# Performance work log

Measured on AMD Instinct MI355X. Metric: run time of the kernel, lower is better.

The kernel has to match this reference:

```python
import jax, jax.numpy as jnp
import numpy as np

N_NODES = 20000
N_EDGES = 320000
N_GRAPHS = 512
HEADS1 = 10
C1 = 78   # per-head out channels of gcn1
C2 = 100  # out channels of gcn2 (heads=1)
NEG_SLOPE = 0.2


def setup_inputs() -> dict:
    key = jax.random.key(0)
    ks = jax.random.split(key, 16)
    glorot = lambda k, shp: jax.random.normal(k, shp, jnp.float32) * np.sqrt(2.0 / (shp[0] + shp[-1]))
    x = jax.random.normal(ks[0], (N_NODES, 78), jnp.float32)
    edge_index = jax.random.randint(ks[1], (2, N_EDGES), 0, N_NODES, jnp.int64)
    batch = jnp.sort(jax.random.randint(ks[2], (N_NODES,), 0, N_GRAPHS, jnp.int64))
    return {
        "x": x,
        "edge_index": edge_index,
        "batch": batch,
        "num_graphs": N_GRAPHS,
        "W1": glorot(ks[3], (78, HEADS1 * C1)),
        "a_src1": glorot(ks[4], (HEADS1, C1)),
        "a_dst1": glorot(ks[5], (HEADS1, C1)),
        "b1": jnp.zeros((HEADS1 * C1,), jnp.float32),
        "W2": glorot(ks[6], (HEADS1 * C1, C2)),
        "a_src2": glorot(ks[7], (1, C2)),
        "a_dst2": glorot(ks[8], (1, C2)),
        "b2": jnp.zeros((C2,), jnp.float32),
        "Wg": glorot(ks[9], (C2, C2)),
        "bg": jnp.zeros((C2,), jnp.float32),
    }


def gat_conv(x, src, dst, W, a_src, a_dst, b, heads, out_ch):
    """PyG-style GATConv (concat=True, add_self_loops already applied, eval mode)."""
    N = x.shape[0]
    h = (x @ W).reshape(N, heads, out_ch)          # [N,H,C]
    alpha_s = jnp.einsum('nhc,hc->nh', h, a_src)   # [N,H]
    alpha_d = jnp.einsum('nhc,hc->nh', h, a_dst)
    e = jax.nn.leaky_relu(alpha_s[src] + alpha_d[dst], NEG_SLOPE)  # [E,H]
    # segment softmax over destination nodes
    m = jax.ops.segment_max(e, dst, num_segments=N)                # [N,H]
    e = jnp.exp(e - m[dst])
    denom = jax.ops.segment_sum(e, dst, num_segments=N)
    alpha = e / (denom[dst] + 1e-16)                               # [E,H]
    out = jax.ops.segment_sum(h[src] * alpha[:, :, None], dst, num_segments=N)
    return out.reshape(N, heads * out_ch) + b


def reference(x, edge_index, batch, num_graphs, W1, a_src1, a_dst1, b1,
              W2, a_src2, a_dst2, b2, Wg, bg):
    N = x.shape[0]
    # add self loops (PyG GATConv default)
    loops = jnp.arange(N, dtype=edge_index.dtype)
    src = jnp.concatenate([edge_index[0], loops])
    dst = jnp.concatenate([edge_index[1], loops])
    h = gat_conv(x, src, dst, W1, a_src1, a_dst1, b1, HEADS1, C1)   # [N,780]
    h = jax.nn.elu(h)
    h = gat_conv(h, src, dst, W2, a_src2, a_dst2, b2, 1, C2)        # [N,100]
    h = jax.nn.relu(h)
    g = jax.ops.segment_max(h, batch, num_segments=num_graphs)      # [G,100] global max pool
    g = jax.nn.relu(g @ Wg + bg)
    return g
```

## Files before the change

### kernel.cpp

```cpp
#include <hip/hip_runtime.h>
#include <hip/hip_bf16.h>

#define N_NODES  20000
#define N_EDGES  320000
#define E_TOT    (N_EDGES + N_NODES)
#define N_GRAPHS 512
#define H1 10
#define C1 78
#define F1 780
#define C2 100
#define NEG_SLOPE 0.2f
#define KSPLIT 5
#define K1PAD 96
#define K2PAD 800
#define K2CHUNK 160
#define AP1 104
#define AP2 40
#define HP 12

typedef short bf16x8 __attribute__((ext_vector_type(8)));
typedef float f32x4 __attribute__((ext_vector_type(4)));
typedef _Float16 half2v __attribute__((ext_vector_type(2)));
typedef unsigned short ushort_t;

__device__ __forceinline__ float bf_lo(unsigned int u) { return __uint_as_float(u << 16); }
__device__ __forceinline__ float bf_hi(unsigned int u) { return __uint_as_float(u & 0xFFFF0000u); }
__device__ __forceinline__ ushort_t f2b(float v) {
  __hip_bfloat16 b = __float2bfloat16(v);
  return *reinterpret_cast<ushort_t*>(&b);
}
__device__ __forceinline__ ushort_t f2h(float v) {
  _Float16 h = (_Float16)v;
  return *reinterpret_cast<ushort_t*>(&h);
}
__device__ __forceinline__ float lrelu(float v) { return (v > 0.f) ? v : NEG_SLOPE * v; }
__device__ __forceinline__ float dot2h(unsigned int a, unsigned int b, float c) {
  union { unsigned int u; half2v v; } A, B;
  A.u = a; B.u = b;
  return __builtin_amdgcn_fdot2(A.v, B.v, c, false);
}


__global__ void k_count(const int* __restrict__ ei, int* __restrict__ cnt) {
  int e = blockIdx.x * blockDim.x + threadIdx.x;
  if (e >= E_TOT) return;
  int dst = (e < N_EDGES) ? ei[N_EDGES + e] : (e - N_EDGES);
  atomicAdd(&cnt[dst], 1);
}

__global__ __launch_bounds__(1024) void k_scan(const int* __restrict__ cnt,
                                               int* __restrict__ offs, int n) {
  const int PER = 20;
  int t = threadIdx.x;
  int lane = t & 63, wv = t >> 6;
  int base = t * PER;
  int loc[PER];
  int run = 0;
#pragma unroll
  for (int k = 0; k < PER; k++) {
    int idx = base + k;
    int v = (idx < n) ? cnt[idx] : 0;
    run += v;
    loc[k] = run;
  }
  int total = run;
  int sc = total;
#pragma unroll
  for (int o = 1; o < 64; o <<= 1) {
    int u = __shfl_up(sc, o);
    if (lane >= o) sc += u;
  }
  __shared__ int ws[16];
  if (lane == 63) ws[wv] = sc;
  __syncthreads();
  if (t == 0) {
    int r = 0;
#pragma unroll
    for (int i = 0; i < 16; i++) { int v = ws[i]; ws[i] = r; r += v; }
  }
  __syncthreads();
  int excl = ws[wv] + sc - total;
#pragma unroll
  for (int k = 0; k < PER; k++) {
    int idx = base + k;
    if (idx < n) offs[idx + 1] = excl + loc[k];
  }
  if (t == 0) offs[0] = 0;
}

__global__ void k_scatter(const int* __restrict__ ei, const int* __restrict__ offs,
                          int* __restrict__ cursor, int* __restrict__ srcs,
                          int* __restrict__ dsts) {
  int e = blockIdx.x * blockDim.x + threadIdx.x;
  if (e >= E_TOT) return;
  int src, dst;
  if (e < N_EDGES) { src = ei[e]; dst = ei[N_EDGES + e]; }
  else             { src = dst = e - N_EDGES; }
  int pos = offs[dst] + atomicAdd(&cursor[dst], 1);
  srcs[pos] = src;
  dsts[pos] = dst;
}


#define PR0 (2 * H1 * C1)
#define PR1 (H1 * 80 * K1PAD)
#define PR2 (112 * K2PAD)
#define PR3 (N_NODES * (K2PAD - F1))
#define PR4 (N_NODES * 40)

__global__ void k_prep(const float* __restrict__ W1, const float* __restrict__ a_src,
                       const float* __restrict__ a_dst, const float* __restrict__ W2,
                       const float* __restrict__ x,
                       float* __restrict__ Vs, float* __restrict__ Vd,
                       ushort_t* __restrict__ W1t, ushort_t* __restrict__ W2t,
                       ushort_t* __restrict__ hab, ushort_t* __restrict__ xhf) {
  int t = blockIdx.x * blockDim.x + threadIdx.x;
  if (t < PR0) {
    int which = (t >= H1 * C1) ? 1 : 0;
    int r = t - which * H1 * C1;
    int h = r / C1, k = r - h * C1;
    const float* a = which ? a_dst : a_src;
    float s = 0.f;
    for (int c = 0; c < C1; c++) s += W1[(size_t)k * F1 + h * C1 + c] * a[h * C1 + c];
    (which ? Vd : Vs)[h * C1 + k] = s;
    return;
  }
  t -= PR0;
  if (t < PR1) {
    int h = t / (80 * K1PAD);
    int rem = t - h * 80 * K1PAD;
    int c = rem / K1PAD, k = rem - c * K1PAD;
    float v = (c < C1 && k < C1) ? W1[(size_t)k * F1 + h * C1 + c] : 0.f;
    W1t[t] = f2b(v);
    return;
  }
  t -= PR1;
  if (t < PR2) {
    int c = t / K2PAD, k = t - c * K2PAD;
    float v = (c < C2 && k < F1) ? W2[(size_t)k * C2 + c] : 0.f;
    W2t[t] = f2b(v);
    return;
  }
  t -= PR2;
  if (t < PR3) {
    int n = t / (K2PAD - F1), j = t - n * (K2PAD - F1);
    hab[(size_t)n * K2PAD + F1 + j] = 0;
    return;
  }
  t -= PR3;
  if (t < PR4) {
    int n = t / 40, c2 = t - n * 40;
    ushort2 o;
    if (c2 < 39) { o.x = f2h(x[(size_t)n * C1 + 2 * c2]); o.y = f2h(x[(size_t)n * C1 + 2 * c2 + 1]); }
    else         { o.x = 0; o.y = 0; }
    *(ushort2*)(xhf + (size_t)n * 80 + 2 * c2) = o;
  }
}


__global__ __launch_bounds__(256) void k_alpha1x(const float* __restrict__ x,
                                                 const float* __restrict__ Vs,
                                                 const float* __restrict__ Vd,
                                                 float* __restrict__ asb,
                                                 float* __restrict__ adb) {
  __shared__ float sVs[H1 * C1], sVd[H1 * C1];
  for (int i = threadIdx.x; i < H1 * C1; i += 256) { sVs[i] = Vs[i]; sVd[i] = Vd[i]; }
  __syncthreads();
  int t = blockIdx.x * 256 + threadIdx.x;
  if (t >= N_NODES * H1) return;
  int n = t / H1, h = t - n * H1;
  const float2* row = (const float2*)(x + (size_t)n * C1);
  const float2* vs2 = (const float2*)(sVs + h * C1);
  const float2* vd2 = (const float2*)(sVd + h * C1);
  float s0 = 0.f, s1 = 0.f;
#pragma unroll 13
  for (int i = 0; i < C1 / 2; i++) {
    float2 v = row[i];
    float2 a = vs2[i];
    float2 b = vd2[i];
    s0 += v.x * a.x + v.y * a.y;
    s1 += v.x * b.x + v.y * b.y;
  }
  asb[(size_t)n * HP + h] = s0;
  adb[(size_t)n * HP + h] = s1;
}


__global__ void k_ex1(const float* __restrict__ asb, const float* __restrict__ adb,
                      const int* __restrict__ srcs, const int* __restrict__ dsts,
                      ushort_t* __restrict__ ex1t) {
  int e = blockIdx.x * blockDim.x + threadIdx.x;
  if (e >= E_TOT) return;
  int s = srcs[e], d = dsts[e];
  const float* pa = asb + (size_t)s * HP;
  const float* pd = adb + (size_t)d * HP;
  float4 a0 = *(const float4*)pa, a1 = *(const float4*)(pa + 4);
  float2 a2 = *(const float2*)(pa + 8);
  float4 d0 = *(const float4*)pd, d1 = *(const float4*)(pd + 4);
  float2 d2 = *(const float2*)(pd + 8);
  float r[10];
  r[0] = __expf(lrelu(a0.x + d0.x)); r[1] = __expf(lrelu(a0.y + d0.y));
  r[2] = __expf(lrelu(a0.z + d0.z)); r[3] = __expf(lrelu(a0.w + d0.w));
  r[4] = __expf(lrelu(a1.x + d1.x)); r[5] = __expf(lrelu(a1.y + d1.y));
  r[6] = __expf(lrelu(a1.z + d1.z)); r[7] = __expf(lrelu(a1.w + d1.w));
  r[8] = __expf(lrelu(a2.x + d2.x)); r[9] = __expf(lrelu(a2.y + d2.y));
#pragma unroll
  for (int h = 0; h < H1; h++) ex1t[(size_t)h * E_TOT + e] = f2h(r[h]);
}


__global__ __launch_bounds__(256) void k_aggv5(const ushort_t* __restrict__ xhf,
                                               const ushort_t* __restrict__ ex1t,
                                               const int* __restrict__ offs,
                                               const int* __restrict__ srcs,
                                               ushort_t* __restrict__ xb) {
  int wid = (blockIdx.x * 256 + threadIdx.x) >> 6;
  int lane = threadIdx.x & 63;
  if (wid >= N_NODES) return;
  int n = wid;
  int beg = __builtin_amdgcn_readfirstlane(offs[n]);
  int end = __builtin_amdgcn_readfirstlane(offs[n + 1]);

  float acc0[H1] = {}, acc1[H1] = {}, sum[H1] = {};
  const unsigned int ONES = 0x3C003C00u;

  for (int e0 = beg & ~1; e0 < end; e0 += 2) {
    unsigned int m = 0xFFFFFFFFu;
    if (e0 < beg) m &= 0xFFFF0000u;
    if (e0 + 1 >= end) m &= 0x0000FFFFu;
    int s0 = srcs[e0], s1 = srcs[e0 + 1];
    unsigned int w[H1];
#pragma unroll
    for (int h = 0; h < H1; h++)
      w[h] = *(const unsigned int*)(ex1t + (size_t)h * E_TOT + e0);
    unsigned int xv0 = 0, xv1 = 0;
    if (lane < 39) {
      xv0 = *(const unsigned int*)(xhf + (size_t)s0 * 80 + 2 * lane);
      xv1 = *(const unsigned int*)(xhf + (size_t)s1 * 80 + 2 * lane);
    }
    unsigned int xA = __builtin_amdgcn_perm(xv1, xv0, 0x05040100u) & m;
    unsigned int xB = __builtin_amdgcn_perm(xv1, xv0, 0x07060302u) & m;
    unsigned int on = ONES & m;
#pragma unroll
    for (int h = 0; h < H1; h++) {
      acc0[h] = dot2h(w[h], xA, acc0[h]);
      acc1[h] = dot2h(w[h], xB, acc1[h]);
      sum[h]  = dot2h(w[h], on, sum[h]);
    }
  }

  if (lane < 48) {
    int colu = (lane < 39) ? 2 * lane : C1 + 2 * (lane - 39);
#pragma unroll
    for (int h = 0; h < H1; h++) {
      float iv = 1.f / (sum[h] + 1e-16f);
      ushort2 o;
      if (lane < 39) { o.x = f2b(acc0[h] * iv); o.y = f2b(acc1[h] * iv); }
      else           { o.x = 0; o.y = 0; }
      *(ushort2*)(xb + ((size_t)h * N_NODES + n) * K1PAD + colu) = o;
    }
  }
}


__global__ __launch_bounds__(256) void k_bgemm_m(const ushort_t* __restrict__ xb,
                                                 const ushort_t* __restrict__ W1t,
                                                 const float* __restrict__ b1,
                                                 ushort_t* __restrict__ hab) {
  __shared__ ushort_t sA[64 * AP1];
  __shared__ ushort_t sB[80 * AP1];
  int h = blockIdx.y;
  int m0 = blockIdx.x * 64;
  int tid = threadIdx.x;

  for (int i = tid; i < 64 * 12; i += 256) {
    int r = i / 12, cx = i - r * 12;
    uint4 v = make_uint4(0, 0, 0, 0);
    int m = m0 + r;
    if (m < N_NODES) v = *(const uint4*)(xb + ((size_t)h * N_NODES + m) * K1PAD + cx * 8);
    *(uint4*)(sA + r * AP1 + cx * 8) = v;
  }
  for (int i = tid; i < 80 * 12; i += 256) {
    int c = i / 12, cx = i - c * 12;
    uint4 v = *(const uint4*)(W1t + ((size_t)h * 80 + c) * K1PAD + cx * 8);
    *(uint4*)(sB + c * AP1 + cx * 8) = v;
  }
  __syncthreads();

  int w = tid >> 6, l = tid & 63;
  int rb = l & 15, g = l >> 4;
  f32x4 acc[5] = {};
  const ushort_t* pa = sA + (w * 16 + rb) * AP1 + g * 8;
#pragma unroll
  for (int k0 = 0; k0 < K1PAD; k0 += 32) {
    bf16x8 a = *(const bf16x8*)(pa + k0);
#pragma unroll
    for (int ct = 0; ct < 5; ct++) {
      bf16x8 b = *(const bf16x8*)(sB + (ct * 16 + rb) * AP1 + k0 + g * 8);
      acc[ct] = __builtin_amdgcn_mfma_f32_16x16x32_bf16(a, b, acc[ct], 0, 0, 0);
    }
  }

  int mrow = m0 + w * 16 + g * 4;
#pragma unroll
  for (int ct = 0; ct < 5; ct++) {
    int col = ct * 16 + rb;
    if (col >= C1) continue;
    float bias = b1[h * C1 + col];
#pragma unroll
    for (int r = 0; r < 4; r++) {
      int m = mrow + r;
      if (m >= N_NODES) continue;
      float v = acc[ct][r] + bias;
      v = (v > 0.f) ? v : (__expf(v) - 1.f);
      hab[(size_t)m * K2PAD + h * C1 + col] = f2b(v);
    }
  }
}


__global__ __launch_bounds__(256) void k_gemm2m(const ushort_t* __restrict__ hab,
                                                const ushort_t* __restrict__ W2t,
                                                float* __restrict__ part) {
  __shared__ ushort_t sA[64 * AP2];
  __shared__ ushort_t sB[112 * AP2];
  int m0 = blockIdx.x * 64;
  int kz = blockIdx.y * K2CHUNK;
  int tid = threadIdx.x;
  int w = tid >> 6, l = tid & 63;
  int rb = l & 15, g = l >> 4;
  f32x4 acc[7] = {};

  for (int ks = 0; ks < K2CHUNK; ks += 32) {
    int kbase = kz + ks;
    {
      int r = tid >> 2, cx = tid & 3;
      uint4 v = make_uint4(0, 0, 0, 0);
      int m = m0 + r;
      if (m < N_NODES) v = *(const uint4*)(hab + (size_t)m * K2PAD + kbase + cx * 8);
      *(uint4*)(sA + r * AP2 + cx * 8) = v;
    }
    for (int i = tid; i < 112 * 4; i += 256) {
      int c = i >> 2, cx = i & 3;
      uint4 v = *(const uint4*)(W2t + (size_t)c * K2PAD + kbase + cx * 8);
      *(uint4*)(sB + c * AP2 + cx * 8) = v;
    }
    __syncthreads();
    bf16x8 a = *(const bf16x8*)(sA + (w * 16 + rb) * AP2 + g * 8);
#pragma unroll
    for (int ct = 0; ct < 7; ct++) {
      bf16x8 b = *(const bf16x8*)(sB + (ct * 16 + rb) * AP2 + g * 8);
      acc[ct] = __builtin_amdgcn_mfma_f32_16x16x32_bf16(a, b, acc[ct], 0, 0, 0);
    }
    __syncthreads();
  }

  float* P = part + (size_t)blockIdx.y * N_NODES * C2;
  int mrow = m0 + w * 16 + g * 4;
#pragma unroll
  for (int ct = 0; ct < 7; ct++) {
    int col = ct * 16 + rb;
    if (col >= C2) continue;
#pragma unroll
    for (int r = 0; r < 4; r++) {
      int m = mrow + r;
      if (m < N_NODES) P[(size_t)m * C2 + col] = acc[ct][r];
    }
  }
}


__global__ __launch_bounds__(256) void k_redalpha(const float* __restrict__ part,
                                                  const float* __restrict__ a_src,
                                                  const float* __restrict__ a_dst,
                                                  ushort_t* __restrict__ z2b,
                                                  float* __restrict__ as2,
                                                  float* __restrict__ ad2) {
  int wid = (blockIdx.x * 256 + threadIdx.x) >> 6;
  int lane = threadIdx.x & 63;
  if (wid >= N_NODES) return;
  float ps = 0.f, pd = 0.f;
  if (lane < C2 / 2) {
    float2 s = make_float2(0.f, 0.f);
#pragma unroll
    for (int c = 0; c < KSPLIT; c++) {
      float2 v = *(const float2*)(part + (size_t)c * N_NODES * C2 + (size_t)wid * C2 + 2 * lane);
      s.x += v.x; s.y += v.y;
    }
    ushort2 o; o.x = f2b(s.x); o.y = f2b(s.y);
    *(ushort2*)(z2b + (size_t)wid * C2 + 2 * lane) = o;
    ps = s.x * a_src[2 * lane] + s.y * a_src[2 * lane + 1];
    pd = s.x * a_dst[2 * lane] + s.y * a_dst[2 * lane + 1];
  }
#pragma unroll
  for (int o = 32; o; o >>= 1) { ps += __shfl_xor(ps, o); pd += __shfl_xor(pd, o); }
  if (lane == 0) { as2[wid] = ps; ad2[wid] = pd; }
}


__global__ void k_ex2(const float* __restrict__ as2, const float* __restrict__ ad2,
                      const int* __restrict__ srcs, const int* __restrict__ dsts,
                      float* __restrict__ ex2) {
  int e = blockIdx.x * blockDim.x + threadIdx.x;
  if (e > E_TOT) return;
  if (e == E_TOT) { ex2[e] = 0.f; return; }
  float v = as2[srcs[e]] + ad2[dsts[e]];
  ex2[e] = __expf(lrelu(v));
}


__global__ __launch_bounds__(256) void k_gat2v3(const ushort_t* __restrict__ z2b,
                                                const float* __restrict__ ex2,
                                                const int* __restrict__ offs,
                                                const int* __restrict__ srcs,
                                                const float* __restrict__ b2,
                                                const int* __restrict__ batch,
                                                unsigned int* __restrict__ pool) {
  int wid = (blockIdx.x * 256 + threadIdx.x) >> 6;
  int lane = threadIdx.x & 63;
  if (wid >= N_NODES) return;
  int n = wid;
  int beg = offs[n], deg = offs[n + 1] - beg;
  const unsigned int* zrow = (const unsigned int*)z2b;

  float acc0 = 0.f, acc1 = 0.f, sum = 0.f;

  for (int j = 0; j < deg; j += 8) {
    int ej[8], sj[8];
#pragma unroll
    for (int q = 0; q < 8; q++) {
      int jj = j + q;
      bool v = jj < deg;
      ej[q] = v ? beg + jj : E_TOT;
      sj[q] = srcs[v ? beg + jj : beg];
    }
    float p[8];
#pragma unroll
    for (int q = 0; q < 8; q++) p[q] = ex2[ej[q]];
    unsigned int z[8] = {0, 0, 0, 0, 0, 0, 0, 0};
    if (lane < C2 / 2) {
#pragma unroll
      for (int q = 0; q < 8; q++) z[q] = zrow[(size_t)sj[q] * (C2 / 2) + lane];
    }
#pragma unroll
    for (int q = 0; q < 8; q++) {
      acc0 += p[q] * bf_lo(z[q]);
      acc1 += p[q] * bf_hi(z[q]);
      sum += p[q];
    }
  }

  if (lane < C2 / 2) {
    float iv = 1.f / (sum + 1e-16f);
    float v0 = fmaxf(acc0 * iv + b2[2 * lane], 0.f);
    float v1 = fmaxf(acc1 * iv + b2[2 * lane + 1], 0.f);
    int g = batch[n];
    atomicMax(&pool[g * C2 + 2 * lane], __float_as_uint(v0));
    atomicMax(&pool[g * C2 + 2 * lane + 1], __float_as_uint(v1));
  }
}


__global__ __launch_bounds__(128) void k_head(const float* __restrict__ pool,
                                              const float* __restrict__ Wg,
                                              const float* __restrict__ bg,
                                              float* __restrict__ out) {
  __shared__ float row[C2];
  int g = blockIdx.x;
  if (threadIdx.x < C2) row[threadIdx.x] = pool[g * C2 + threadIdx.x];
  __syncthreads();
  int c = threadIdx.x;
  if (c < C2) {
    float acc = bg[c];
    for (int k = 0; k < C2; k++) acc += row[k] * Wg[k * C2 + c];
    out[g * C2 + c] = fmaxf(acc, 0.f);
  }
}


extern "C" void kernel_launch(void* const* d_in, const int* in_sizes, int n_in,
                              void* d_out, int out_size, void* d_ws, size_t ws_size,
                              hipStream_t stream) {
  const float* x      = (const float*)d_in[0];
  const int*   ei     = (const int*)d_in[1];
  const int*   batch  = (const int*)d_in[2];
  const float* W1     = (const float*)d_in[4];
  const float* a_src1 = (const float*)d_in[5];
  const float* a_dst1 = (const float*)d_in[6];
  const float* b1     = (const float*)d_in[7];
  const float* W2     = (const float*)d_in[8];
  const float* a_src2 = (const float*)d_in[9];
  const float* a_dst2 = (const float*)d_in[10];
  const float* b2     = (const float*)d_in[11];
  const float* Wg     = (const float*)d_in[12];
  const float* bg     = (const float*)d_in[13];
  float* out = (float*)d_out;

  char* w = (char*)d_ws;
  size_t off = 0;
  auto alloc = [&](size_t bytes) -> void* {
    void* p = w + off;
    off += (bytes + 255) & ~(size_t)255;
    return p;
  };

  ushort_t* xb   = (ushort_t*)alloc((size_t)H1 * N_NODES * K1PAD * 2);
  ushort_t* hab  = (ushort_t*)alloc((size_t)N_NODES * K2PAD * 2);
  float* part    = (float*)alloc((size_t)KSPLIT * N_NODES * C2 * 4);
  float* asb     = (float*)alloc((size_t)N_NODES * HP * 4);
  float* adb     = (float*)alloc((size_t)N_NODES * HP * 4);
  ushort_t* ex1t = (ushort_t*)alloc((size_t)H1 * E_TOT * 2);
  ushort_t* xhf  = (ushort_t*)alloc((size_t)N_NODES * 80 * 2);
  float* Vs      = (float*)alloc((size_t)H1 * C1 * 4);
  float* Vd      = (float*)alloc((size_t)H1 * C1 * 4);
  ushort_t* W1t  = (ushort_t*)alloc((size_t)H1 * 80 * K1PAD * 2);
  ushort_t* W2t  = (ushort_t*)alloc((size_t)112 * K2PAD * 2);
  int* cnt           = (int*)alloc((size_t)N_NODES * 4);
  int* cursor        = (int*)alloc((size_t)N_NODES * 4);
  unsigned int* pool = (unsigned int*)alloc((size_t)N_GRAPHS * C2 * 4);
  size_t zspan = (size_t)((char*)(pool + (size_t)N_GRAPHS * C2) - (char*)cnt);
  int* offs   = (int*)alloc((size_t)(N_NODES + 1) * 4);
  int* srcs   = (int*)alloc((size_t)E_TOT * 4);
  int* dsts   = (int*)alloc((size_t)E_TOT * 4);

  float* as2    = (float*)xb;
  float* ad2    = as2 + N_NODES;
  ushort_t* z2b = (ushort_t*)(ad2 + N_NODES);
  float* ex2    = (float*)(z2b + (size_t)N_NODES * C2);

  hipMemsetAsync(cnt, 0, zspan, stream);

  k_count<<<(E_TOT + 255) / 256, 256, 0, stream>>>(ei, cnt);
  k_scan<<<1, 1024, 0, stream>>>(cnt, offs, N_NODES);
  k_scatter<<<(E_TOT + 255) / 256, 256, 0, stream>>>(ei, offs, cursor, srcs, dsts);

  k_prep<<<(PR0 + PR1 + PR2 + PR3 + PR4 + 255) / 256, 256, 0, stream>>>(
      W1, a_src1, a_dst1, W2, x, Vs, Vd, W1t, W2t, hab, xhf);
  k_alpha1x<<<(N_NODES * H1 + 255) / 256, 256, 0, stream>>>(x, Vs, Vd, asb, adb);
  k_ex1<<<(E_TOT + 255) / 256, 256, 0, stream>>>(asb, adb, srcs, dsts, ex1t);
  k_aggv5<<<(N_NODES + 3) / 4, 256, 0, stream>>>(xhf, ex1t, offs, srcs, xb);
  k_bgemm_m<<<dim3((N_NODES + 63) / 64, H1), 256, 0, stream>>>(xb, W1t, b1, hab);

  k_gemm2m<<<dim3((N_NODES + 63) / 64, KSPLIT), 256, 0, stream>>>(hab, W2t, part);
  k_redalpha<<<(N_NODES + 3) / 4, 256, 0, stream>>>(part, a_src2, a_dst2, z2b, as2, ad2);
  k_ex2<<<(E_TOT + 1 + 255) / 256, 256, 0, stream>>>(as2, ad2, srcs, dsts, ex2);
  k_gat2v3<<<(N_NODES + 3) / 4, 256, 0, stream>>>(z2b, ex2, offs, srcs, b2, batch, pool);
  k_head<<<N_GRAPHS, 128, 0, stream>>>((const float*)pool, Wg, bg, out);
}
```

Measured before the change: 275.6 us.

## Merge count/prep and scan/alpha kernels; fold edge exp into layer-2 aggregation

```diff
diff --git a/kernel.cpp b/kernel.cpp
--- a/kernel.cpp
+++ b/kernel.cpp
@@ -41,80 +41,31 @@
 }
 
 
-__global__ void k_count(const int* __restrict__ ei, int* __restrict__ cnt) {
-  int e = blockIdx.x * blockDim.x + threadIdx.x;
-  if (e >= E_TOT) return;
-  int dst = (e < N_EDGES) ? ei[N_EDGES + e] : (e - N_EDGES);
-  atomicAdd(&cnt[dst], 1);
-}
-
-__global__ __launch_bounds__(1024) void k_scan(const int* __restrict__ cnt,
-                                               int* __restrict__ offs, int n) {
-  const int PER = 20;
-  int t = threadIdx.x;
-  int lane = t & 63, wv = t >> 6;
-  int base = t * PER;
-  int loc[PER];
-  int run = 0;
-#pragma unroll
-  for (int k = 0; k < PER; k++) {
-    int idx = base + k;
-    int v = (idx < n) ? cnt[idx] : 0;
-    run += v;
-    loc[k] = run;
-  }
-  int total = run;
-  int sc = total;
-#pragma unroll
-  for (int o = 1; o < 64; o <<= 1) {
-    int u = __shfl_up(sc, o);
-    if (lane >= o) sc += u;
-  }
-  __shared__ int ws[16];
-  if (lane == 63) ws[wv] = sc;
-  __syncthreads();
-  if (t == 0) {
-    int r = 0;
-#pragma unroll
-    for (int i = 0; i < 16; i++) { int v = ws[i]; ws[i] = r; r += v; }
-  }
-  __syncthreads();
-  int excl = ws[wv] + sc - total;
-#pragma unroll
-  for (int k = 0; k < PER; k++) {
-    int idx = base + k;
-    if (idx < n) offs[idx + 1] = excl + loc[k];
-  }
-  if (t == 0) offs[0] = 0;
-}
-
-__global__ void k_scatter(const int* __restrict__ ei, const int* __restrict__ offs,
-                          int* __restrict__ cursor, int* __restrict__ srcs,
-                          int* __restrict__ dsts) {
-  int e = blockIdx.x * blockDim.x + threadIdx.x;
-  if (e >= E_TOT) return;
-  int src, dst;
-  if (e < N_EDGES) { src = ei[e]; dst = ei[N_EDGES + e]; }
-  else             { src = dst = e - N_EDGES; }
-  int pos = offs[dst] + atomicAdd(&cursor[dst], 1);
-  srcs[pos] = src;
-  dsts[pos] = dst;
-}
-
-
 #define PR0 (2 * H1 * C1)
 #define PR1 (H1 * 80 * K1PAD)
 #define PR2 (112 * K2PAD)
 #define PR3 (N_NODES * (K2PAD - F1))
 #define PR4 (N_NODES * 40)
-
-__global__ void k_prep(const float* __restrict__ W1, const float* __restrict__ a_src,
-                       const float* __restrict__ a_dst, const float* __restrict__ W2,
-                       const float* __restrict__ x,
-                       float* __restrict__ Vs, float* __restrict__ Vd,
-                       ushort_t* __restrict__ W1t, ushort_t* __restrict__ W2t,
-                       ushort_t* __restrict__ hab, ushort_t* __restrict__ xhf) {
-  int t = blockIdx.x * blockDim.x + threadIdx.x;
+#define PRT (PR0 + PR1 + PR2 + PR3 + PR4)
+#define NB_CNT ((E_TOT + 255) / 256)
+#define NB_PREP ((PRT + 255) / 256)
+
+__global__ void k_cntprep(const int* __restrict__ ei,
+                          const float* __restrict__ W1, const float* __restrict__ a_src,
+                          const float* __restrict__ a_dst, const float* __restrict__ W2,
+                          const float* __restrict__ x,
+                          int* __restrict__ cnt,
+                          float* __restrict__ Vs, float* __restrict__ Vd,
+                          ushort_t* __restrict__ W1t, ushort_t* __restrict__ W2t,
+                          ushort_t* __restrict__ hab, ushort_t* __restrict__ xhf) {
+  if (blockIdx.x < NB_CNT) {
+    int e = blockIdx.x * 256 + threadIdx.x;
+    if (e >= E_TOT) return;
+    int dst = (e < N_EDGES) ? ei[N_EDGES + e] : (e - N_EDGES);
+    atomicAdd(&cnt[dst], 1);
+    return;
+  }
+  int t = (blockIdx.x - NB_CNT) * 256 + threadIdx.x;
   if (t < PR0) {
     int which = (t >= H1 * C1) ? 1 : 0;
     int r = t - which * H1 * C1;
@@ -158,15 +109,63 @@
 }
 
 
-__global__ __launch_bounds__(256) void k_alpha1x(const float* __restrict__ x,
-                                                 const float* __restrict__ Vs,
-                                                 const float* __restrict__ Vd,
-                                                 float* __restrict__ asb,
-                                                 float* __restrict__ adb) {
+__global__ __launch_bounds__(1024) void k_scanalpha(const int* __restrict__ cnt,
+                                                    int* __restrict__ offs,
+                                                    const float* __restrict__ x,
+                                                    const float* __restrict__ Vs,
+                                                    const float* __restrict__ Vd,
+                                                    float* __restrict__ asb,
+                                                    float* __restrict__ adb) {
+  if (blockIdx.x == 0) {
+    const int PER = 20;
+    int t = threadIdx.x;
+    int lane = t & 63, wv = t >> 6;
+    int base = t * PER;
+    int raw[PER];
+    const int4* c4 = (const int4*)(cnt + base);
+#pragma unroll
+    for (int q = 0; q < 5; q++) {
+      int4 v = c4[q];
+      raw[4 * q] = v.x; raw[4 * q + 1] = v.y; raw[4 * q + 2] = v.z; raw[4 * q + 3] = v.w;
+    }
+    int loc[PER];
+    int run = 0;
+#pragma unroll
+    for (int k = 0; k < PER; k++) {
+      int idx = base + k;
+      run += (idx < N_NODES) ? raw[k] : 0;
+      loc[k] = run;
+    }
+    int total = run;
+    int sc = total;
+#pragma unroll
+    for (int o = 1; o < 64; o <<= 1) {
+      int u = __shfl_up(sc, o);
+      if (lane >= o) sc += u;
+    }
+    __shared__ int ws[16];
+    if (lane == 63) ws[wv] = sc;
+    __syncthreads();
+    if (t == 0) {
+      int r = 0;
+#pragma unroll
+      for (int i = 0; i < 16; i++) { int v = ws[i]; ws[i] = r; r += v; }
+    }
+    __syncthreads();
+    int excl = ws[wv] + sc - total;
+#pragma unroll
+    for (int k = 0; k < PER; k++) {
+      int idx = base + k;
+      if (idx < N_NODES) offs[idx + 1] = excl + loc[k];
+    }
+    if (t == 0) offs[0] = 0;
+    return;
+  }
+
   __shared__ float sVs[H1 * C1], sVd[H1 * C1];
-  for (int i = threadIdx.x; i < H1 * C1; i += 256) { sVs[i] = Vs[i]; sVd[i] = Vd[i]; }
+  for (int i = threadIdx.x; i < H1 * C1; i += 1024) { sVs[i] = Vs[i]; sVd[i] = Vd[i]; }
   __syncthreads();
-  int t = blockIdx.x * 256 + threadIdx.x;
+  int t = (blockIdx.x - 1) * 1024 + threadIdx.x;
   if (t >= N_NODES * H1) return;
   int n = t / H1, h = t - n * H1;
   const float2* row = (const float2*)(x + (size_t)n * C1);
@@ -183,6 +182,19 @@
   }
   asb[(size_t)n * HP + h] = s0;
   adb[(size_t)n * HP + h] = s1;
+}
+
+__global__ void k_scatter(const int* __restrict__ ei, const int* __restrict__ offs,
+                          int* __restrict__ cursor, int* __restrict__ srcs,
+                          int* __restrict__ dsts) {
+  int e = blockIdx.x * blockDim.x + threadIdx.x;
+  if (e >= E_TOT) return;
+  int src, dst;
+  if (e < N_EDGES) { src = ei[e]; dst = ei[N_EDGES + e]; }
+  else             { src = dst = e - N_EDGES; }
+  int pos = offs[dst] + atomicAdd(&cursor[dst], 1);
+  srcs[pos] = src;
+  dsts[pos] = dst;
 }
 
 
@@ -398,19 +410,9 @@
 }
 
 
-__global__ void k_ex2(const float* __restrict__ as2, const float* __restrict__ ad2,
-                      const int* __restrict__ srcs, const int* __restrict__ dsts,
-                      float* __restrict__ ex2) {
-  int e = blockIdx.x * blockDim.x + threadIdx.x;
-  if (e > E_TOT) return;
-  if (e == E_TOT) { ex2[e] = 0.f; return; }
-  float v = as2[srcs[e]] + ad2[dsts[e]];
-  ex2[e] = __expf(lrelu(v));
-}
-
-
-__global__ __launch_bounds__(256) void k_gat2v3(const ushort_t* __restrict__ z2b,
-                                                const float* __restrict__ ex2,
+__global__ __launch_bounds__(256) void k_gat2v4(const ushort_t* __restrict__ z2b,
+                                                const float* __restrict__ as2,
+                                                const float* __restrict__ ad2,
                                                 const int* __restrict__ offs,
                                                 const int* __restrict__ srcs,
                                                 const float* __restrict__ b2,
@@ -421,22 +423,25 @@
   if (wid >= N_NODES) return;
   int n = wid;
   int beg = offs[n], deg = offs[n + 1] - beg;
+  float adn = ad2[n];
   const unsigned int* zrow = (const unsigned int*)z2b;
 
   float acc0 = 0.f, acc1 = 0.f, sum = 0.f;
 
   for (int j = 0; j < deg; j += 8) {
-    int ej[8], sj[8];
+    int sj[8]; bool vj[8];
 #pragma unroll
     for (int q = 0; q < 8; q++) {
       int jj = j + q;
-      bool v = jj < deg;
-      ej[q] = v ? beg + jj : E_TOT;
-      sj[q] = srcs[v ? beg + jj : beg];
+      vj[q] = jj < deg;
+      sj[q] = srcs[vj[q] ? beg + jj : beg];
     }
     float p[8];
 #pragma unroll
-    for (int q = 0; q < 8; q++) p[q] = ex2[ej[q]];
+    for (int q = 0; q < 8; q++) {
+      float pv = __expf(lrelu(as2[sj[q]] + adn));
+      p[q] = vj[q] ? pv : 0.f;
+    }
     unsigned int z[8] = {0, 0, 0, 0, 0, 0, 0, 0};
     if (lane < C2 / 2) {
 #pragma unroll
@@ -526,24 +531,20 @@
   float* as2    = (float*)xb;
   float* ad2    = as2 + N_NODES;
   ushort_t* z2b = (ushort_t*)(ad2 + N_NODES);
-  float* ex2    = (float*)(z2b + (size_t)N_NODES * C2);
 
   hipMemsetAsync(cnt, 0, zspan, stream);
 
-  k_count<<<(E_TOT + 255) / 256, 256, 0, stream>>>(ei, cnt);
-  k_scan<<<1, 1024, 0, stream>>>(cnt, offs, N_NODES);
+  k_cntprep<<<NB_CNT + NB_PREP, 256, 0, stream>>>(ei, W1, a_src1, a_dst1, W2, x,
+                                                  cnt, Vs, Vd, W1t, W2t, hab, xhf);
+  k_scanalpha<<<1 + (N_NODES * H1 + 1023) / 1024, 1024, 0, stream>>>(cnt, offs, x, Vs, Vd,
+                                                                     asb, adb);
   k_scatter<<<(E_TOT + 255) / 256, 256, 0, stream>>>(ei, offs, cursor, srcs, dsts);
-
-  k_prep<<<(PR0 + PR1 + PR2 + PR3 + PR4 + 255) / 256, 256, 0, stream>>>(
-      W1, a_src1, a_dst1, W2, x, Vs, Vd, W1t, W2t, hab, xhf);
-  k_alpha1x<<<(N_NODES * H1 + 255) / 256, 256, 0, stream>>>(x, Vs, Vd, asb, adb);
   k_ex1<<<(E_TOT + 255) / 256, 256, 0, stream>>>(asb, adb, srcs, dsts, ex1t);
   k_aggv5<<<(N_NODES + 3) / 4, 256, 0, stream>>>(xhf, ex1t, offs, srcs, xb);
   k_bgemm_m<<<dim3((N_NODES + 63) / 64, H1), 256, 0, stream>>>(xb, W1t, b1, hab);
 
   k_gemm2m<<<dim3((N_NODES + 63) / 64, KSPLIT), 256, 0, stream>>>(hab, W2t, part);
   k_redalpha<<<(N_NODES + 3) / 4, 256, 0, stream>>>(part, a_src2, a_dst2, z2b, as2, ad2);
-  k_ex2<<<(E_TOT + 1 + 255) / 256, 256, 0, stream>>>(as2, ad2, srcs, dsts, ex2);
-  k_gat2v3<<<(N_NODES + 3) / 4, 256, 0, stream>>>(z2b, ex2, offs, srcs, b2, batch, pool);
+  k_gat2v4<<<(N_NODES + 3) / 4, 256, 0, stream>>>(z2b, as2, ad2, offs, srcs, b2, batch, pool);
   k_head<<<N_GRAPHS, 128, 0, stream>>>((const float*)pool, Wg, bg, out);
 }
```

Result: faster. 255.5 us (-7.3%).
